# Kernel optimization log

Hardware: AMD Instinct MI355X
Metric: run time of the kernel (lower is better)

Reference implementation:

```python
import jax, jax.numpy as jnp
import numpy as np

K = 3          # kernel_size
PAD = K // 2   # padding applied before deform conv


def setup_inputs() -> dict:
    key = jax.random.key(0)
    ks = jax.random.split(key, 5)
    B, C, H, W = 4, 64, 64, 256
    O = 64  # out_channels
    x = jax.random.normal(ks[0], (B, C, H, W), jnp.float32)
    # offset conv params (torch Conv2d default init scale ~ 1/sqrt(fan_in) ~ 0.04)
    offset_w = jax.random.normal(ks[1], (2 * K * K, C, K, K), jnp.float32) * 0.04
    offset_b = jax.random.normal(ks[2], (2 * K * K,), jnp.float32) * 0.04
    # original module uses torch.rand (uniform [0,1)) for weight and mask
    weight = jax.random.uniform(ks[3], (O, C, K, K), jnp.float32)
    mask = jax.random.uniform(ks[4], (B, K * K, H, W), jnp.float32)
    return dict(x=x, offset_w=offset_w, offset_b=offset_b, weight=weight, mask=mask)


def _trianglewave(x):
    n = jnp.floor(x / np.pi + 0.5)
    sign = 1.0 - 2.0 * jnp.mod(n, 2.0)  # (-1)**n for integer-valued float n
    return (x - np.pi * n) * sign


def prak(x):
    # preluconst = 1.0
    return _trianglewave(x) + _trianglewave(x + np.pi / 2)


def deform_conv2d(xp, offsets, weight, mask):
    # xp: [B,C,Hp,Wp] padded input; offsets: [B,2*K*K,H,W]; weight: [O,C,K,K]; mask: [B,K*K,H,W]
    B, C, Hp, Wp = xp.shape
    H, W = offsets.shape[2], offsets.shape[3]
    P = K * K
    off = offsets.reshape(B, P, 2, H, W)
    off_y, off_x = off[:, :, 0], off[:, :, 1]
    ii = (jnp.arange(P) // K).astype(jnp.float32)  # kernel row per tap p
    jj = (jnp.arange(P) % K).astype(jnp.float32)   # kernel col per tap p
    base_y = jnp.arange(H, dtype=jnp.float32)[None, :, None] + ii[:, None, None]  # [P,H,1]
    base_x = jnp.arange(W, dtype=jnp.float32)[None, None, :] + jj[:, None, None]  # [P,1,W]
    py = base_y[None] + off_y  # [B,P,H,W] sampling rows (stride=1, no extra pad)
    px = base_x[None] + off_x
    y0 = jnp.floor(py)
    x0 = jnp.floor(px)
    flat = xp.reshape(B, C, Hp * Wp)

    def gather(yc, xc):
        valid = (yc >= 0) & (yc <= Hp - 1) & (xc >= 0) & (xc <= Wp - 1)
        yi = jnp.clip(yc, 0, Hp - 1).astype(jnp.int32)
        xi = jnp.clip(xc, 0, Wp - 1).astype(jnp.int32)
        idx = (yi * Wp + xi).reshape(B, 1, -1)  # [B,1,P*H*W]
        v = jnp.take_along_axis(flat, jnp.broadcast_to(idx, (B, C, idx.shape[-1])), axis=2)
        return v.reshape(B, C, P, H, W) * valid.astype(xp.dtype).reshape(B, 1, P, H, W)

    wy1 = py - y0
    wx1 = px - x0
    wy0 = 1.0 - wy1
    wx0 = 1.0 - wx1
    val = (gather(y0, x0) * (wy0 * wx0)[:, None]
           + gather(y0, x0 + 1) * (wy0 * wx1)[:, None]
           + gather(y0 + 1, x0) * (wy1 * wx0)[:, None]
           + gather(y0 + 1, x0 + 1) * (wy1 * wx1)[:, None])  # [B,C,P,H,W]
    val = val * mask[:, None]  # modulation mask
    O = weight.shape[0]
    return jnp.einsum('ocp,bcphw->bohw', weight.reshape(O, C, P), val)


def reference(x, offset_w, offset_b, weight, mask):
    # x: [B,C,H,W]
    x_addon = jax.lax.stop_gradient(x)  # x.detach() branch
    xp = jnp.pad(x, ((0, 0), (0, 0), (PAD, PAD), (PAD, PAD)))
    offsets = jax.lax.conv_general_dilated(
        xp, offset_w, (1, 1), 'VALID',
        dimension_numbers=('NCHW', 'OIHW', 'NCHW')) + offset_b[None, :, None, None]
    y = deform_conv2d(xp, offsets, weight, mask)  # [B,O,H,W]
    # F.layer_norm with normalized_shape == full tensor shape: global mean/var, no affine
    mu = jnp.mean(y)
    var = jnp.mean((y - mu) ** 2)
    y = (y - mu) * jax.lax.rsqrt(var + 1e-5)
    y = prak(y)
    y = jnp.concatenate([y, x_addon], axis=1)  # [B,O+C,H,W]
    # MaxPool2d(kernel_size=K, stride=2), VALID padding
    out = jax.lax.reduce_window(y, -jnp.inf, jax.lax.max,
                                (1, 1, K, K), (1, 1, 2, 2), 'VALID')
    return out
```

## Files before the change

### kernel.cpp

```cpp
#include <hip/hip_runtime.h>
#include <math.h>

#define BN 4
#define CN 64
#define HN 64
#define WN 256
#define ON 64
#define NOC 18
#define PN 9
#define HO 31
#define WO 127

#define VST 584
#define VSB 1168

typedef __attribute__((ext_vector_type(8))) short bf16x8;
typedef __attribute__((ext_vector_type(4))) float f32x4;

__device__ __forceinline__ unsigned short f2bf(float f) {
    unsigned int u = __float_as_uint(f);
    unsigned int r = (u + 0x7fffu + ((u >> 16) & 1u)) >> 16;
    return (unsigned short)r;
}

__device__ __forceinline__ unsigned int cvtpk(float lo, float hi) {
    unsigned int r;
    asm("v_cvt_pk_bf16_f32 %0, %1, %2" : "=v"(r) : "v"(lo), "v"(hi));
    return r;
}

__device__ __forceinline__ float trianglewave(float x) {
    const float PI_F = 3.14159274101257324f;
    float n = floorf(x / PI_F + 0.5f);
    float m = fmodf(n, 2.0f);
    if (m < 0.0f) m += 2.0f;
    float sgn = 1.0f - 2.0f * m;
    return (x - PI_F * n) * sgn;
}

__device__ __forceinline__ float prak_f(float x) {
    const float PI_HALF = 1.57079637050628662f;
    return trianglewave(x) + trianglewave(x + PI_HALF);
}

__global__ __launch_bounds__(512) void prep_transpose_kernel(
        const float* __restrict__ x,
        const float* __restrict__ offw,
        const float* __restrict__ wgt,
        unsigned short* __restrict__ xt,
        unsigned short* __restrict__ Wf,
        unsigned short* __restrict__ WoF) {
    if (blockIdx.x < 512) {
        __shared__ float Tl[128][65];
        int blk = blockIdx.x;
        int whalf = blk & 1;
        int h = (blk >> 1) & 63;
        int b = blk >> 7;
        int t = threadIdx.x;
        int fq = t & 31;
#pragma unroll
        for (int j = 0; j < 4; j++) {
            int c = (t >> 5) + 16 * j;
            float4 v = *(const float4*)(x + ((size_t)(b * CN + c) * HN + h) * WN + whalf * 128 + fq * 4);
            Tl[fq * 4 + 0][c] = v.x;
            Tl[fq * 4 + 1][c] = v.y;
            Tl[fq * 4 + 2][c] = v.z;
            Tl[fq * 4 + 3][c] = v.w;
        }
        __syncthreads();
        int cq = t & 7;
#pragma unroll
        for (int j = 0; j < 2; j++) {
            int wl = (t >> 3) + 64 * j;
            uint4 pk;
            pk.x = cvtpk(Tl[wl][cq * 8 + 0], Tl[wl][cq * 8 + 1]);
            pk.y = cvtpk(Tl[wl][cq * 8 + 2], Tl[wl][cq * 8 + 3]);
            pk.z = cvtpk(Tl[wl][cq * 8 + 4], Tl[wl][cq * 8 + 5]);
            pk.w = cvtpk(Tl[wl][cq * 8 + 6], Tl[wl][cq * 8 + 7]);
            *(uint4*)(xt + (((size_t)(b * HN) + h) * WN + whalf * 128 + wl) * 64 + cq * 8) = pk;
        }
    } else {
        int t = (blockIdx.x - 512) * 512 + threadIdx.x;
        if (t < 4 * 18 * 64 * 8) {
            int j    = t & 7;
            int lane = (t >> 3) & 63;
            int rest = t >> 9;
            int ks   = rest % 18;
            int m    = rest / 18;
            int o = m * 16 + (lane & 15);
            int k = ks * 32 + (lane >> 4) * 8 + j;
            int c = k & 63;
            int p = k >> 6;
            Wf[t] = f2bf(wgt[(o * CN + c) * 9 + p]);
        }
        if (t < 2 * 18 * 64 * 8) {
            int j    = t & 7;
            int lane = (t >> 3) & 63;
            int rest = t >> 9;
            int ks   = rest % 18;
            int mo   = rest / 18;
            int o = mo * 16 + (lane & 15);
            int k = ks * 32 + (lane >> 4) * 8 + j;
            int c = k & 63;
            int p = k >> 6;
            WoF[t] = (o < NOC) ? f2bf(offw[(o * CN + c) * 9 + p]) : (unsigned short)0;
        }
    }
}

struct TapS { float w00, w01, w10, w11; int a0, a1, a2, a3; };

__global__ __launch_bounds__(512, 4) void fused_kernel(
        const unsigned short* __restrict__ xt,
        const float* __restrict__ offb,
        const float* __restrict__ mask,
        const unsigned short* __restrict__ WoF,
        const unsigned short* __restrict__ Wf,
        float* __restrict__ y,
        float2* __restrict__ partials) {
    __shared__ __align__(16) unsigned short V[64 * VST];
    __shared__ float offs_lds[NOC * 64];
    __shared__ float red1[8], red2[8];

    int bid = blockIdx.x;
    int logical = ((bid & 7) << 7) + (bid >> 3);
    int b = logical >> 8;
    int h = (logical >> 2) & 63;
    int wblk = logical & 3;
    int lane = threadIdx.x & 63;
    int wv = threadIdx.x >> 6;

    int pl = threadIdx.x >> 3;
    int cg = threadIdx.x & 7;
    int w = (wblk << 6) + pl;
    const unsigned short* xb = xt + (size_t)b * HN * WN * 64;
    const uint4* xb4 = (const uint4*)xb;
    int kq = lane >> 4;

#pragma unroll
    for (int p = 0; p < PN; p++) {
        int iy = h + p / 3 - 1;
        int ix = w + p % 3 - 1;
        uint4 pk = {0u, 0u, 0u, 0u};
        if (iy >= 0 && iy < HN && ix >= 0 && ix < WN)
            pk = xb4[((size_t)iy * WN + ix) * 8 + cg];
        *(uint4*)((char*)V + pl * VSB + p * 128 + cg * 16) = pk;
    }
    __syncthreads();

    {
        int mo = wv >> 2;
        int nt = wv & 3;
        f32x4 acc = {0.0f, 0.0f, 0.0f, 0.0f};
        const bf16x8* Wov = (const bf16x8*)WoF;
        int pixc = nt * 16 + (lane & 15);
#pragma unroll
        for (int ks = 0; ks < 18; ks++) {
            bf16x8 a = Wov[(mo * 18 + ks) * 64 + lane];
            bf16x8 bfr = *(const bf16x8*)((char*)V + pixc * VSB + ks * 64 + kq * 16);
            acc = __builtin_amdgcn_mfma_f32_16x16x32_bf16(a, bfr, acc, 0, 0, 0);
        }
        int ocb = mo * 16 + kq * 4;
#pragma unroll
        for (int r = 0; r < 4; r++) {
            int oc = ocb + r;
            if (oc < NOC) offs_lds[oc * 64 + pixc] = acc[r] + offb[oc];
        }
    }
    __syncthreads();

    {
        float mkv[9];
#pragma unroll
        for (int p = 0; p < 9; p++) mkv[p] = mask[((b * PN + p) * HN + h) * WN + w];

        auto stage = [&](int p) -> TapS {
            TapS s;
            float offy = offs_lds[(2 * p) * 64 + pl];
            float offx = offs_lds[(2 * p + 1) * 64 + pl];
            float mk = mkv[p];
            float py = (float)(h + p / 3) + offy;
            float px = (float)(w + p % 3) + offx;
            float fy0 = floorf(py), fx0 = floorf(px);
            float wy1 = py - fy0, wx1 = px - fx0;
            float wy0 = 1.0f - wy1, wx0 = 1.0f - wx1;
            int iy0 = (int)fy0 - 1, ix0 = (int)fx0 - 1;
            int iy1 = iy0 + 1, ix1 = ix0 + 1;
            bool vy0 = (iy0 >= 0) && (iy0 < HN);
            bool vy1 = (iy1 >= 0) && (iy1 < HN);
            bool vx0 = (ix0 >= 0) && (ix0 < WN);
            bool vx1 = (ix1 >= 0) && (ix1 < WN);
            s.w00 = (vy0 && vx0) ? wy0 * wx0 * mk : 0.0f;
            s.w01 = (vy0 && vx1) ? wy0 * wx1 * mk : 0.0f;
            s.w10 = (vy1 && vx0) ? wy1 * wx0 * mk : 0.0f;
            s.w11 = (vy1 && vx1) ? wy1 * wx1 * mk : 0.0f;
            int cy0 = min(max(iy0, 0), HN - 1), cy1 = min(max(iy1, 0), HN - 1);
            int cx0 = min(max(ix0, 0), WN - 1), cx1 = min(max(ix1, 0), WN - 1);
            s.a0 = (cy0 * WN + cx0) * 8 + cg;
            s.a1 = (cy0 * WN + cx1) * 8 + cg;
            s.a2 = (cy1 * WN + cx0) * 8 + cg;
            s.a3 = (cy1 * WN + cx1) * 8 + cg;
            return s;
        };

        TapS sC = stage(0);
        uint4 A = xb4[sC.a0], B = xb4[sC.a1], C = xb4[sC.a2], D = xb4[sC.a3];

#pragma unroll
        for (int p = 0; p < 9; p++) {
            TapS sN;
            uint4 nA, nB, nC, nD;
            if (p < 8) {
                sN = stage(p + 1);
                nA = xb4[sN.a0]; nB = xb4[sN.a1];
                nC = xb4[sN.a2]; nD = xb4[sN.a3];
            }
            float fa[8], fb[8], fc[8], fd[8];
            {
                unsigned int ua[4] = {A.x, A.y, A.z, A.w};
                unsigned int ub[4] = {B.x, B.y, B.z, B.w};
                unsigned int uc[4] = {C.x, C.y, C.z, C.w};
                unsigned int ud[4] = {D.x, D.y, D.z, D.w};
#pragma unroll
                for (int j = 0; j < 4; j++) {
                    fa[2 * j] = __uint_as_float(ua[j] << 16);
                    fa[2 * j + 1] = __uint_as_float(ua[j] & 0xffff0000u);
                    fb[2 * j] = __uint_as_float(ub[j] << 16);
                    fb[2 * j + 1] = __uint_as_float(ub[j] & 0xffff0000u);
                    fc[2 * j] = __uint_as_float(uc[j] << 16);
                    fc[2 * j + 1] = __uint_as_float(uc[j] & 0xffff0000u);
                    fd[2 * j] = __uint_as_float(ud[j] << 16);
                    fd[2 * j + 1] = __uint_as_float(ud[j] & 0xffff0000u);
                }
            }
            float v[8];
#pragma unroll
            for (int j = 0; j < 8; j++)
                v[j] = sC.w00 * fa[j] + sC.w01 * fb[j] + sC.w10 * fc[j] + sC.w11 * fd[j];
            uint4 pk;
            pk.x = cvtpk(v[0], v[1]);
            pk.y = cvtpk(v[2], v[3]);
            pk.z = cvtpk(v[4], v[5]);
            pk.w = cvtpk(v[6], v[7]);
            *(uint4*)((char*)V + pl * VSB + p * 128 + cg * 16) = pk;
            if (p < 8) {
                sC = sN;
                A = nA; B = nB; C = nC; D = nD;
            }
        }
    }
    __syncthreads();

    int m = wv >> 1;
    int npair = wv & 1;
    f32x4 acc0 = {0.0f, 0.0f, 0.0f, 0.0f};
    f32x4 acc1 = {0.0f, 0.0f, 0.0f, 0.0f};
    const bf16x8* Wfv = (const bf16x8*)Wf;
    int pixc = npair * 32 + (lane & 15);
#pragma unroll
    for (int ks = 0; ks < 18; ks++) {
        bf16x8 a  = Wfv[(m * 18 + ks) * 64 + lane];
        bf16x8 b0 = *(const bf16x8*)((char*)V + pixc * VSB + ks * 64 + kq * 16);
        bf16x8 b1 = *(const bf16x8*)((char*)V + (pixc + 16) * VSB + ks * 64 + kq * 16);
        acc0 = __builtin_amdgcn_mfma_f32_16x16x32_bf16(a, b0, acc0, 0, 0, 0);
        acc1 = __builtin_amdgcn_mfma_f32_16x16x32_bf16(a, b1, acc1, 0, 0, 0);
    }

    int orow = m * 16 + kq * 4;
    float s1 = 0.0f, s2 = 0.0f;
#pragma unroll
    for (int r = 0; r < 4; r++) {
        float v0 = acc0[r];
        float v1 = acc1[r];
        size_t base = (((size_t)(b * ON + orow + r) * HN) + h) * WN + (wblk << 6);
        y[base + pixc] = v0;
        y[base + pixc + 16] = v1;
        s1 += v0 + v1;
        s2 += v0 * v0 + v1 * v1;
    }
#pragma unroll
    for (int off = 32; off > 0; off >>= 1) {
        s1 += __shfl_down(s1, off);
        s2 += __shfl_down(s2, off);
    }
    if (lane == 0) { red1[wv] = s1; red2[wv] = s2; }
    __syncthreads();
    if (threadIdx.x == 0) {
        float t1 = 0.0f, t2 = 0.0f;
#pragma unroll
        for (int i = 0; i < 8; i++) { t1 += red1[i]; t2 += red2[i]; }
        partials[blockIdx.x] = make_float2(t1, t2);
    }
}

__global__ __launch_bounds__(256) void stats_kernel(const float2* __restrict__ partials,
                                                    int nblocks,
                                                    float* __restrict__ stats) {
    __shared__ double r1[256], r2[256];
    int tid = threadIdx.x;
    double s1 = 0.0, s2 = 0.0;
    for (int i = tid; i < nblocks; i += 256) {
        s1 += (double)partials[i].x;
        s2 += (double)partials[i].y;
    }
    r1[tid] = s1;
    r2[tid] = s2;
    __syncthreads();
    for (int s = 128; s > 0; s >>= 1) {
        if (tid < s) { r1[tid] += r1[tid + s]; r2[tid] += r2[tid + s]; }
        __syncthreads();
    }
    if (tid == 0) {
        double N = (double)BN * ON * HN * WN;
        double mu = r1[0] / N;
        double var = r2[0] / N - mu * mu;
        stats[0] = (float)mu;
        stats[1] = (float)(1.0 / sqrt(var + 1e-5));
    }
}

__global__ __launch_bounds__(256) void out_kernel(const float* __restrict__ yb,
                                                  const float* __restrict__ x,
                                                  const float* __restrict__ stats,
                                                  float* __restrict__ out) {
    int t = blockIdx.x * 256 + threadIdx.x;
    if (t >= BN * 128 * HO * WO) return;
    int ow = t % WO;
    int oh = (t / WO) % HO;
    int ch = (t / (WO * HO)) % 128;
    int b  = t / (WO * HO * 128);

    float mu = stats[0];
    float inv = stats[1];
    float m = -INFINITY;
    if (ch < 64) {
        const float* yc = yb + ((size_t)(b * ON + ch) * HN) * WN;
#pragma unroll
        for (int dy = 0; dy < 3; dy++) {
            const float* row = yc + (2 * oh + dy) * WN + 2 * ow;
#pragma unroll
            for (int dx = 0; dx < 3; dx++) {
                float v = prak_f((row[dx] - mu) * inv);
                m = fmaxf(m, v);
            }
        }
    } else {
        const float* xc = x + ((size_t)(b * CN + (ch - 64)) * HN) * WN;
#pragma unroll
        for (int dy = 0; dy < 3; dy++) {
            const float* row = xc + (2 * oh + dy) * WN + 2 * ow;
#pragma unroll
            for (int dx = 0; dx < 3; dx++) m = fmaxf(m, row[dx]);
        }
    }
    out[t] = m;
}

extern "C" void kernel_launch(void* const* d_in, const int* in_sizes, int n_in,
                              void* d_out, int out_size, void* d_ws, size_t ws_size,
                              hipStream_t stream) {
    const float* x    = (const float*)d_in[0];
    const float* offw = (const float*)d_in[1];
    const float* offb = (const float*)d_in[2];
    const float* wgt  = (const float*)d_in[3];
    const float* mask = (const float*)d_in[4];
    float* out = (float*)d_out;

    unsigned short* Wf  = (unsigned short*)d_ws;
    unsigned short* WoF = Wf + 36864;
    float* y  = (float*)(WoF + 18432);
    unsigned short* xt = (unsigned short*)(y + 4194304);
    float2* partials = (float2*)(xt + 4194304);
    float* stats = (float*)(partials + 1024);

    prep_transpose_kernel<<<584, 512, 0, stream>>>(x, offw, wgt, xt, Wf, WoF);
    fused_kernel<<<1024, 512, 0, stream>>>(xt, offb, mask, WoF, Wf, y, partials);
    stats_kernel<<<1, 256, 0, stream>>>(partials, 1024, stats);
    out_kernel<<<7874, 256, 0, stream>>>(y, x, stats, out);
}
```

Baseline: 59.16 us.

## Fold stats reduction into fused kernel, vectorize maxpool, raise MFMA priority

Drops the separate stats kernel: the last block to finish, found with an atomic counter and a threadfence, reduces the per-block partial sums and writes mean and inverse std, saving one launch. The output kernel now has each thread compute four adjacent pooled outputs from shared row loads with float2 vector reads, so it needs fewer threads and loads. s_setprio is raised around the MFMA loops. A memset of the counter is added to every launch, and the last-block reduction runs serially at the tail of the fused kernel.

```diff
diff --git a/kernel.cpp b/kernel.cpp
--- a/kernel.cpp
+++ b/kernel.cpp
@@ -117,10 +117,13 @@
         const unsigned short* __restrict__ WoF,
         const unsigned short* __restrict__ Wf,
         float* __restrict__ y,
-        float2* __restrict__ partials) {
+        float2* __restrict__ partials,
+        float* __restrict__ stats,
+        unsigned int* __restrict__ counter) {
     __shared__ __align__(16) unsigned short V[64 * VST];
     __shared__ float offs_lds[NOC * 64];
     __shared__ float red1[8], red2[8];
+    __shared__ int amLast;
 
     int bid = blockIdx.x;
     int logical = ((bid & 7) << 7) + (bid >> 3);
@@ -154,12 +157,14 @@
         f32x4 acc = {0.0f, 0.0f, 0.0f, 0.0f};
         const bf16x8* Wov = (const bf16x8*)WoF;
         int pixc = nt * 16 + (lane & 15);
+        __builtin_amdgcn_s_setprio(1);
 #pragma unroll
         for (int ks = 0; ks < 18; ks++) {
             bf16x8 a = Wov[(mo * 18 + ks) * 64 + lane];
             bf16x8 bfr = *(const bf16x8*)((char*)V + pixc * VSB + ks * 64 + kq * 16);
             acc = __builtin_amdgcn_mfma_f32_16x16x32_bf16(a, bfr, acc, 0, 0, 0);
         }
+        __builtin_amdgcn_s_setprio(0);
         int ocb = mo * 16 + kq * 4;
 #pragma unroll
         for (int r = 0; r < 4; r++) {
@@ -257,6 +262,7 @@
     f32x4 acc1 = {0.0f, 0.0f, 0.0f, 0.0f};
     const bf16x8* Wfv = (const bf16x8*)Wf;
     int pixc = npair * 32 + (lane & 15);
+    __builtin_amdgcn_s_setprio(1);
 #pragma unroll
     for (int ks = 0; ks < 18; ks++) {
         bf16x8 a  = Wfv[(m * 18 + ks) * 64 + lane];
@@ -265,6 +271,7 @@
         acc0 = __builtin_amdgcn_mfma_f32_16x16x32_bf16(a, b0, acc0, 0, 0, 0);
         acc1 = __builtin_amdgcn_mfma_f32_16x16x32_bf16(a, b1, acc1, 0, 0, 0);
     }
+    __builtin_amdgcn_s_setprio(0);
 
     int orow = m * 16 + kq * 4;
     float s1 = 0.0f, s2 = 0.0f;
@@ -289,33 +296,40 @@
         float t1 = 0.0f, t2 = 0.0f;
 #pragma unroll
         for (int i = 0; i < 8; i++) { t1 += red1[i]; t2 += red2[i]; }
-        partials[blockIdx.x] = make_float2(t1, t2);
-    }
-}
-
-__global__ __launch_bounds__(256) void stats_kernel(const float2* __restrict__ partials,
-                                                    int nblocks,
-                                                    float* __restrict__ stats) {
-    __shared__ double r1[256], r2[256];
-    int tid = threadIdx.x;
-    double s1 = 0.0, s2 = 0.0;
-    for (int i = tid; i < nblocks; i += 256) {
-        s1 += (double)partials[i].x;
-        s2 += (double)partials[i].y;
-    }
-    r1[tid] = s1;
-    r2[tid] = s2;
+        partials[bid] = make_float2(t1, t2);
+        __threadfence();
+        unsigned int old = atomicAdd(counter, 1u);
+        amLast = (old == 1023u) ? 1 : 0;
+    }
     __syncthreads();
-    for (int s = 128; s > 0; s >>= 1) {
-        if (tid < s) { r1[tid] += r1[tid + s]; r2[tid] += r2[tid + s]; }
+
+    if (amLast) {
+        double* dr1 = (double*)V;
+        double* dr2 = (double*)(V + 2048);
+        int tid = threadIdx.x;
+        if (tid < 256) {
+            double a1 = 0.0, a2 = 0.0;
+            for (int i = tid; i < 1024; i += 256) {
+                float px = __hip_atomic_load(&partials[i].x, __ATOMIC_RELAXED, __HIP_MEMORY_SCOPE_AGENT);
+                float py = __hip_atomic_load(&partials[i].y, __ATOMIC_RELAXED, __HIP_MEMORY_SCOPE_AGENT);
+                a1 += (double)px;
+                a2 += (double)py;
+            }
+            dr1[tid] = a1;
+            dr2[tid] = a2;
+        }
         __syncthreads();
-    }
-    if (tid == 0) {
-        double N = (double)BN * ON * HN * WN;
-        double mu = r1[0] / N;
-        double var = r2[0] / N - mu * mu;
-        stats[0] = (float)mu;
-        stats[1] = (float)(1.0 / sqrt(var + 1e-5));
+        for (int s = 128; s > 0; s >>= 1) {
+            if (tid < s) { dr1[tid] += dr1[tid + s]; dr2[tid] += dr2[tid + s]; }
+            __syncthreads();
+        }
+        if (tid == 0) {
+            double N = (double)BN * ON * HN * WN;
+            double mu = dr1[0] / N;
+            double var = dr2[0] / N - mu * mu;
+            stats[0] = (float)mu;
+            stats[1] = (float)(1.0 / sqrt(var + 1e-5));
+        }
     }
 }
 
@@ -324,36 +338,46 @@
                                                   const float* __restrict__ stats,
                                                   float* __restrict__ out) {
     int t = blockIdx.x * 256 + threadIdx.x;
-    if (t >= BN * 128 * HO * WO) return;
-    int ow = t % WO;
-    int oh = (t / WO) % HO;
-    int ch = (t / (WO * HO)) % 128;
-    int b  = t / (WO * HO * 128);
+    int q  = t & 31;
+    int r  = t >> 5;
+    int oh = r % 31;
+    int cr = r / 31;
+    int ch = cr & 127;
+    int b  = cr >> 7;
 
     float mu = stats[0];
     float inv = stats[1];
-    float m = -INFINITY;
-    if (ch < 64) {
-        const float* yc = yb + ((size_t)(b * ON + ch) * HN) * WN;
-#pragma unroll
-        for (int dy = 0; dy < 3; dy++) {
-            const float* row = yc + (2 * oh + dy) * WN + 2 * ow;
-#pragma unroll
-            for (int dx = 0; dx < 3; dx++) {
-                float v = prak_f((row[dx] - mu) * inv);
-                m = fmaxf(m, v);
-            }
-        }
-    } else {
-        const float* xc = x + ((size_t)(b * CN + (ch - 64)) * HN) * WN;
-#pragma unroll
-        for (int dy = 0; dy < 3; dy++) {
-            const float* row = xc + (2 * oh + dy) * WN + 2 * ow;
-#pragma unroll
-            for (int dx = 0; dx < 3; dx++) m = fmaxf(m, row[dx]);
-        }
-    }
-    out[t] = m;
+    float m0 = -INFINITY, m1 = -INFINITY, m2 = -INFINITY, m3 = -INFINITY;
+    const float* plane = (ch < 64)
+        ? yb + ((size_t)(b * ON + ch) * HN) * WN
+        : x + ((size_t)(b * CN + (ch - 64)) * HN) * WN;
+    bool doPrak = (ch < 64);
+
+#pragma unroll
+    for (int dy = 0; dy < 3; dy++) {
+        const float* row = plane + (2 * oh + dy) * WN + 8 * q;
+        float2 r0 = *(const float2*)(row + 0);
+        float2 r1 = *(const float2*)(row + 2);
+        float2 r2 = *(const float2*)(row + 4);
+        float2 r3 = *(const float2*)(row + 6);
+        float  e8 = row[8];
+        float e[9] = {r0.x, r0.y, r1.x, r1.y, r2.x, r2.y, r3.x, r3.y, e8};
+        if (doPrak) {
+#pragma unroll
+            for (int i = 0; i < 9; i++) e[i] = prak_f((e[i] - mu) * inv);
+        }
+        m0 = fmaxf(m0, fmaxf(fmaxf(e[0], e[1]), e[2]));
+        m1 = fmaxf(m1, fmaxf(fmaxf(e[2], e[3]), e[4]));
+        m2 = fmaxf(m2, fmaxf(fmaxf(e[4], e[5]), e[6]));
+        m3 = fmaxf(m3, fmaxf(fmaxf(e[6], e[7]), e[8]));
+    }
+
+    int ow0 = q * 4;
+    size_t obase = (((size_t)(b * 128 + ch) * HO) + oh) * WO + ow0;
+    out[obase + 0] = m0;
+    out[obase + 1] = m1;
+    out[obase + 2] = m2;
+    if (ow0 + 3 < WO) out[obase + 3] = m3;
 }
 
 extern "C" void kernel_launch(void* const* d_in, const int* in_sizes, int n_in,
@@ -372,9 +396,10 @@
     unsigned short* xt = (unsigned short*)(y + 4194304);
     float2* partials = (float2*)(xt + 4194304);
     float* stats = (float*)(partials + 1024);
-
+    unsigned int* counter = (unsigned int*)(stats + 2);
+
+    hipMemsetAsync(counter, 0, sizeof(unsigned int), stream);
     prep_transpose_kernel<<<584, 512, 0, stream>>>(x, offw, wgt, xt, Wf, WoF);
-    fused_kernel<<<1024, 512, 0, stream>>>(xt, offb, mask, WoF, Wf, y, partials);
-    stats_kernel<<<1, 256, 0, stream>>>(partials, 1024, stats);
-    out_kernel<<<7874, 256, 0, stream>>>(y, x, stats, out);
-}
+    fused_kernel<<<1024, 512, 0, stream>>>(xt, offb, mask, WoF, Wf, y, partials, stats, counter);
+    out_kernel<<<1984, 256, 0, stream>>>(y, x, stats, out);
+}
```

Result: slower. 96.97 us (+63.9%).
